# Kernel tuning notes

Hardware: AMD Instinct MI355X
Metric: run time of the kernel (lower is better)

Reference implementation:

```python
import jax, jax.numpy as jnp
import numpy as np

N_NODES = 170
SEQ = 12
BATCH = 32
D_MODEL = 120
N_HEADS = 8
FF_DIM = 2048
K_CHEB = 3  # K=2 -> K+1 = 3 polynomial orders
LN_EPS = 1e-5


def _layer_norm(x, g, b):
    m = jnp.mean(x, -1, keepdims=True)
    v = jnp.mean((x - m) ** 2, -1, keepdims=True)
    return (x - m) * jax.lax.rsqrt(v + LN_EPS) * g + b


def _graph_learn(adj, beta, w1, w2, cw, cb):
    # learned antisymmetric adjacency + 1x1-conv gating + double sym-normalization
    n = adj.shape[0]
    eps = 0.5 / n
    new = jax.nn.relu(w1 @ w2.T - w2 @ w1.T + jnp.diag(beta))
    gate = jax.nn.sigmoid(cw[0] * new + cw[1] * adj + cb)  # Conv2d(2,1,1) == weighted sum
    a = gate * new + (1.0 - gate) * adj
    d = jax.lax.rsqrt(jnp.sum(a, 1))
    a = jax.nn.relu(d[:, None] * a * d[None, :] - eps)
    d = jax.lax.rsqrt(jnp.sum(a, 1))
    return d[:, None] * a * d[None, :]


def _cheb_conv(x2d, graph, w, b):
    # x2d: (B*T, N, C); graph: (N, N); w: (K, C, O); b: (O,)
    n = graph.shape[0]
    d = jax.lax.rsqrt(jnp.sum(graph, -1))
    eye = jnp.eye(n, dtype=x2d.dtype)
    L = eye - d[:, None] * graph * d[None, :]
    Ts = [eye, L]
    for _ in range(w.shape[0] - 2):
        Ts.append(2.0 * (L @ Ts[-1]) - Ts[-2])
    T = jnp.stack(Ts)  # (K, N, N)
    h = jnp.einsum('knm,bmc->kbnc', T, x2d)
    return jnp.einsum('kbnc,kco->bno', h, w) + b


def setup_inputs() -> dict:
    key = jax.random.key(0)
    ks = jax.random.split(key, 16)
    D, F = D_MODEL, FF_DIM
    kaiming = 1.0 / np.sqrt(D)  # kaiming_uniform(a=sqrt(5)) bound for fan_in=D
    xavier = float(np.sqrt(2.0 / (D + D)))
    return {
        'x': jax.random.normal(ks[0], (BATCH, SEQ, N_NODES, D), jnp.float32),
        'adj': jax.random.uniform(ks[1], (N_NODES, N_NODES), jnp.float32),
        # GraphLearn params, stacked for Q/K/V branches (leading dim 3)
        'gl_beta': jax.random.uniform(ks[2], (3, N_NODES), jnp.float32),
        'gl_w1': jax.random.uniform(ks[3], (3, N_NODES, D), jnp.float32, -kaiming, kaiming),
        'gl_w2': jax.random.uniform(ks[4], (3, N_NODES, D), jnp.float32, -kaiming, kaiming),
        'gl_cw': jax.random.normal(ks[5], (3, 2), jnp.float32) * 0.5,
        'gl_cb': jnp.zeros((3,), jnp.float32),
        # ChebConv params per branch
        'cheb_w': jax.random.normal(ks[6], (3, K_CHEB, D, D), jnp.float32) * xavier,
        'cheb_b': jnp.zeros((3, D), jnp.float32),
        # output projection + FFN + layernorms
        'out_w': jax.random.normal(ks[7], (D, D), jnp.float32) / np.sqrt(D),
        'out_b': jnp.zeros((D,), jnp.float32),
        'ff_w1': jax.random.normal(ks[8], (D, F), jnp.float32) / np.sqrt(D),
        'ff_b1': jnp.zeros((F,), jnp.float32),
        'ff_w2': jax.random.normal(ks[9], (F, D), jnp.float32) / np.sqrt(F),
        'ff_b2': jnp.zeros((D,), jnp.float32),
        'ln1_g': jnp.ones((D,), jnp.float32),
        'ln1_b': jnp.zeros((D,), jnp.float32),
        'ln2_g': jnp.ones((D,), jnp.float32),
        'ln2_b': jnp.zeros((D,), jnp.float32),
    }


def reference(x, adj, gl_beta, gl_w1, gl_w2, gl_cw, gl_cb, cheb_w, cheb_b,
              out_w, out_b, ff_w1, ff_b1, ff_w2, ff_b2, ln1_g, ln1_b, ln2_g, ln2_b):
    B, T, N, D = x.shape
    H = N_HEADS
    hd = D // H
    x2d = x.reshape(B * T, N, D)
    qkv = []
    for i in range(3):  # Q, K, V branches (structurally distinct params)
        g = _graph_learn(adj, gl_beta[i], gl_w1[i], gl_w2[i], gl_cw[i], gl_cb[i])
        g = jax.lax.stop_gradient(g)  # torch code does graph.clone().detach()
        h = jax.nn.relu(_cheb_conv(x2d, g, cheb_w[i], cheb_b[i]))
        qkv.append(h.reshape(B, T, N, D))
    q, k, v = qkv

    def to_heads(t):  # (B,T,N,D) -> (B,N,T,H,hd)
        return t.transpose(0, 2, 1, 3).reshape(B, N, T, H, hd)
    q, k, v = to_heads(q), to_heads(k), to_heads(v)
    scores = jnp.einsum('bnqhd,bnkhd->bnhqk', q, k) / (hd ** 0.5)
    attn = jax.nn.softmax(scores, axis=-1)
    o = jnp.einsum('bnhqk,bnkhd->bnqhd', attn, v).reshape(B, N, T, D)
    o = o @ out_w + out_b  # (B,N,T,D)
    out = _layer_norm(x + o.transpose(0, 2, 1, 3), ln1_g, ln1_b)  # residual in (B,T,N,D)
    ff = jax.nn.relu(out @ ff_w1 + ff_b1) @ ff_w2 + ff_b2
    out = _layer_norm(out + ff, ln2_g, ln2_b)
    return out
```

## Files before the change

### kernel.cpp

```cpp
#include <hip/hip_runtime.h>
#include <cstddef>
#include <cstdint>

#define N_NODES 170
#define SEQ 12
#define BATCH 32
#define DM 120
#define BT (BATCH*SEQ)
#define ROWS (BT*N_NODES)
#define FF 2048

typedef short short8 __attribute__((ext_vector_type(8)));
typedef float f32x4 __attribute__((ext_vector_type(4)));

static constexpr size_t OFF_A    = 0;
static constexpr size_t OFF_G    = 86704;
static constexpr size_t OFF_A2   = 173408;
static constexpr size_t OFF_L    = 260112;
static constexpr size_t OFF_RS1  = 307824;
static constexpr size_t OFF_RS2  = 308336;
static constexpr size_t OFF_RS3  = 308848;
static constexpr size_t OFF_XT   = 309360;
static constexpr size_t OFF_XNM  = OFF_XT  + 4325376;
static constexpr size_t OFF_Y1T  = OFF_XNM + 4177920;
static constexpr size_t OFF_YNM  = OFF_Y1T + 3*4325376;
static constexpr size_t OFF_BC   = OFF_YNM + 3*8355840;
static constexpr size_t OFF_HQ   = OFF_XT;
static constexpr size_t OFF_HK   = OFF_Y1T;
static constexpr size_t OFF_HV   = OFF_Y1T + 4177920;
static constexpr size_t OFF_W1T  = OFF_YNM;
static constexpr size_t OFF_W2R  = OFF_W1T + 131072;
static constexpr size_t OFF_ONM  = OFF_W2R + 131072;
static constexpr size_t OFF_LN1  = OFF_ONM + 4177920;
static constexpr size_t OFF_LN1B = OFF_LN1 + 7833600;
static constexpr size_t OFF_OWT  = OFF_LN1B + 4177920;

static constexpr size_t Y1T_BR_STRIDE = 8650752;
static constexpr size_t YNM_BR_STRIDE = 16711680;

__device__ __forceinline__ unsigned short f2bf(float f) {
    unsigned int u = __float_as_uint(f);
    unsigned int r = (u + 0x7fffu + ((u >> 16) & 1u)) >> 16;
    return (unsigned short)r;
}
__device__ __forceinline__ float bf2f(unsigned short h) {
    return __uint_as_float(((unsigned int)h) << 16);
}
__device__ __forceinline__ void gld16(const void* g, void* l) {
    __builtin_amdgcn_global_load_lds(
        (const __attribute__((address_space(1))) void*)g,
        (__attribute__((address_space(3))) void*)l, 16, 0, 0);
}
__device__ __forceinline__ uint4 pack8(const unsigned short v[8]) {
    uint4 q;
    q.x = (unsigned)v[0] | ((unsigned)v[1] << 16);
    q.y = (unsigned)v[2] | ((unsigned)v[3] << 16);
    q.z = (unsigned)v[4] | ((unsigned)v[5] << 16);
    q.w = (unsigned)v[6] | ((unsigned)v[7] << 16);
    return q;
}

__global__ __launch_bounds__(256)
void k_gl1(const float* __restrict__ adj, const float* __restrict__ beta,
           const float* __restrict__ w1, const float* __restrict__ w2,
           const float* __restrict__ cw, const float* __restrict__ cb,
           float* __restrict__ a_out, float* __restrict__ rs_out) {
    int i  = blockIdx.x;
    int br = blockIdx.y;
    __shared__ float w1r[DM], w2r[DM];
    __shared__ float red[256];
    int tid = threadIdx.x;
    const float* w1b = w1 + (size_t)br * N_NODES * DM;
    const float* w2b = w2 + (size_t)br * N_NODES * DM;
    if (tid < DM) {
        w1r[tid] = w1b[(size_t)i * DM + tid];
        w2r[tid] = w2b[(size_t)i * DM + tid];
    }
    __syncthreads();
    float aval = 0.f;
    if (tid < N_NODES) {
        int j = tid;
        const float4* w1j = (const float4*)(w1b + (size_t)j * DM);
        const float4* w2j = (const float4*)(w2b + (size_t)j * DM);
        float s1 = 0.f, s2 = 0.f;
#pragma unroll 6
        for (int cc = 0; cc < DM / 4; ++cc) {
            float4 u = w2j[cc];
            float4 v = w1j[cc];
            s1 += w1r[cc*4+0]*u.x + w1r[cc*4+1]*u.y + w1r[cc*4+2]*u.z + w1r[cc*4+3]*u.w;
            s2 += w2r[cc*4+0]*v.x + w2r[cc*4+1]*v.y + w2r[cc*4+2]*v.z + w2r[cc*4+3]*v.w;
        }
        float nv = s1 - s2 + (j == i ? beta[br * N_NODES + i] : 0.f);
        nv = fmaxf(nv, 0.f);
        float adjv = adj[(size_t)i * N_NODES + j];
        float z = cw[br*2+0] * nv + cw[br*2+1] * adjv + cb[br];
        float gate = 1.f / (1.f + __expf(-z));
        aval = gate * nv + (1.f - gate) * adjv;
        a_out[((size_t)br * N_NODES + i) * N_NODES + j] = aval;
    }
    red[tid] = aval;
    __syncthreads();
    for (int s = 128; s > 0; s >>= 1) {
        if (tid < s) red[tid] += red[tid + s];
        __syncthreads();
    }
    if (tid == 0) rs_out[br * N_NODES + i] = red[0];
}

__global__ __launch_bounds__(256)
void k_glnorm(const float* __restrict__ in, const float* __restrict__ rs,
              float* __restrict__ out, float* __restrict__ rs_out, int mode) {
    int i  = blockIdx.x;
    int br = blockIdx.y;
    __shared__ float red[256];
    int tid = threadIdx.x;
    float di = rsqrtf(rs[br * N_NODES + i]);
    float contrib = 0.f;
    if (tid < N_NODES) {
        float dj = rsqrtf(rs[br * N_NODES + tid]);
        float v = di * in[((size_t)br * N_NODES + i) * N_NODES + tid] * dj;
        float o;
        if (mode == 2) { o = fmaxf(v - 0.5f / 170.f, 0.f); contrib = o; }
        else           { o = v; contrib = v; }
        out[((size_t)br * N_NODES + i) * N_NODES + tid] = o;
    }
    red[tid] = contrib;
    __syncthreads();
    for (int s = 128; s > 0; s >>= 1) {
        if (tid < s) red[tid] += red[tid + s];
        __syncthreads();
    }
    if (tid == 0) rs_out[br * N_NODES + i] = red[0];
}

__global__ __launch_bounds__(192)
void k_prep_L(const float* __restrict__ g_buf, const float* __restrict__ rs3,
              unsigned short* __restrict__ Lbf) {
    int i  = blockIdx.x;
    int br = blockIdx.y;
    int j  = threadIdx.x;
    if (j >= 180) return;
    float v = 0.f;
    if (i < N_NODES && j < N_NODES) {
        float di = rsqrtf(rs3[br * N_NODES + i]);
        float dj = rsqrtf(rs3[br * N_NODES + j]);
        float gg = g_buf[((size_t)br * N_NODES + i) * N_NODES + j];
        v = (i == j ? 1.f : 0.f) - di * gg * dj;
    }
    Lbf[(size_t)br * 31808 + i * 180 + j] = f2bf(v);
}

__global__ __launch_bounds__(256)
void k_prep_x(const float* __restrict__ x, unsigned short* __restrict__ xTF,
              unsigned short* __restrict__ xnm) {
    __shared__ unsigned short LX[170 * 121 + 8];
    int bt = blockIdx.x, tid = threadIdx.x;
    const float* xb = x + (size_t)bt * N_NODES * DM;
    for (int u = tid; u < 170 * 30; u += 256) {
        int nn = u / 30, cq = u - nn * 30;
        float4 v = *(const float4*)&xb[nn * 120 + cq * 4];
        LX[nn * 121 + cq * 4 + 0] = f2bf(v.x);
        LX[nn * 121 + cq * 4 + 1] = f2bf(v.y);
        LX[nn * 121 + cq * 4 + 2] = f2bf(v.z);
        LX[nn * 121 + cq * 4 + 3] = f2bf(v.w);
    }
    __syncthreads();
    for (int u = tid; u < 128 * 22; u += 256) {
        int c = u / 22, mb = u - c * 22;
        unsigned short vals[8];
#pragma unroll
        for (int i2 = 0; i2 < 8; ++i2) {
            int m = mb * 8 + i2;
            vals[i2] = (c < 120 && m < 170) ? LX[m * 121 + c] : (unsigned short)0;
        }
        *(uint4*)&xTF[(size_t)bt * 22528 + ((size_t)mb * 128 + c) * 8] = pack8(vals);
    }
    for (int u = tid; u < 170 * 16; u += 256) {
        int nn = u >> 4, b = u & 15;
        unsigned int row = bt * 170 + nn;
        unsigned short vals[8];
#pragma unroll
        for (int i2 = 0; i2 < 8; ++i2) {
            int c = b * 8 + i2;
            vals[i2] = (c < 120) ? LX[nn * 121 + c] : (unsigned short)0;
        }
        int bs = (b & 8) | ((b & 7) ^ (row & 7));
        *(uint4*)&xnm[(size_t)row * 128 + bs * 8] = pack8(vals);
    }
}

__global__ __launch_bounds__(256)
void k_prep_Bc(const float* __restrict__ cheb_w, unsigned short* __restrict__ Bc) {
    int idx = blockIdx.x * 256 + threadIdx.x;
    int br  = idx / 49152;
    int rem = idx - br * 49152;
    int o   = rem / 384;
    int c   = rem - o * 384;
    float v = 0.f;
    if (o < 120) {
        int part = c >> 7, cc = c & 127;
        if (cc < 120) {
            const float* Wb = cheb_w + (size_t)br * 3 * 14400;
            if (part == 0)      v = Wb[cc * 120 + o] - Wb[2 * 14400 + cc * 120 + o];
            else if (part == 1) v = Wb[14400 + cc * 120 + o];
            else                v = 2.f * Wb[2 * 14400 + cc * 120 + o];
        }
    }
    Bc[(size_t)br * 49152 + (((size_t)(c >> 3) * 128 + o) << 3) + (c & 7)] = f2bf(v);
}

__global__ __launch_bounds__(256)
void k_lapplyT(const unsigned short* __restrict__ Asrc_base, size_t asrc_br_stride,
               const unsigned short* __restrict__ Lg_base,
               unsigned short* __restrict__ yT_base,
               unsigned short* __restrict__ ynm_base, int coloff) {
    __shared__ __attribute__((aligned(16))) unsigned short Llds[31744];
    const int tid = threadIdx.x, w = tid >> 6, lane = tid & 63;
    const int g = lane >> 4, l15 = lane & 15;
    const int bt = blockIdx.x, br = blockIdx.y;
    const unsigned short* Asrc = Asrc_base + (size_t)br * asrc_br_stride + (size_t)bt * 22528;
    const unsigned short* Lg   = Lg_base + (size_t)br * 31808;
    unsigned short* ynm = ynm_base + (size_t)br * YNM_BR_STRIDE;
    unsigned short* yT  = yT_base ? yT_base + (size_t)br * Y1T_BR_STRIDE + (size_t)bt * 22528 : nullptr;
    const char* Lgb = (const char*)Lg;
    char* Lldsb = (char*)Llds;
#pragma unroll
    for (int it = 0; it < 16; ++it) {
        int q = it * 4 + w;
        if (q * 1024 < 63360)
            gld16(Lgb + q * 1024 + lane * 16, Lldsb + q * 1024);
    }
    short8 af[2][6];
#pragma unroll
    for (int ct2 = 0; ct2 < 2; ++ct2) {
        int c = (w * 2 + ct2) * 16 + l15;
#pragma unroll
        for (int kb = 0; kb < 6; ++kb) {
            if (kb < 5) af[ct2][kb] = *(const short8*)&Asrc[(((size_t)(kb * 4 + g)) * 128 + c) * 8];
            else {
                short8 z = {};
                af[ct2][kb] = (g < 2) ? *(const short8*)&Asrc[(((size_t)(20 + g)) * 128 + c) * 8] : z;
            }
        }
    }
    __syncthreads();
    f32x4 acc[2][11];
#pragma unroll
    for (int a = 0; a < 2; ++a)
#pragma unroll
        for (int b = 0; b < 11; ++b) acc[a][b] = (f32x4){0.f, 0.f, 0.f, 0.f};
#pragma unroll
    for (int kb = 0; kb < 6; ++kb) {
#pragma unroll
        for (int nt = 0; nt < 11; ++nt) {
            short8 bf;
            int rb = (nt * 16 + l15) * 180;
            if (kb < 5) bf = *(const short8*)&Llds[rb + kb * 32 + g * 8];
            else {
                short8 z = {};
                bf = (g < 2) ? *(const short8*)&Llds[rb + 160 + g * 8] : z;
            }
            acc[0][nt] = __builtin_amdgcn_mfma_f32_16x16x32_bf16(af[0][kb], bf, acc[0][nt], 0, 0, 0);
            acc[1][nt] = __builtin_amdgcn_mfma_f32_16x16x32_bf16(af[1][kb], bf, acc[1][nt], 0, 0, 0);
        }
    }
#pragma unroll
    for (int nt = 0; nt < 11; ++nt) {
        int nn = nt * 16 + l15;
#pragma unroll
        for (int ct2 = 0; ct2 < 2; ++ct2) {
            int base_c = (w * 2 + ct2) * 16 + g * 4;
            if (yT) {
                int f = nn >> 3, j = nn & 7;
#pragma unroll
                for (int r = 0; r < 4; ++r) {
                    int c = base_c + r;
                    float v = (c < 120 && nn < 170) ? acc[ct2][nt][r] : 0.f;
                    yT[(((size_t)f * 128 + c) << 3) + j] = f2bf(v);
                }
            }
            if (nn < 170) {
                unsigned int row = bt * 170 + nn;
                unsigned short u[4];
#pragma unroll
                for (int r = 0; r < 4; ++r)
                    u[r] = (base_c + r < 120) ? f2bf(acc[ct2][nt][r]) : (unsigned short)0;
                int bc  = coloff + base_c;
                int blk = bc >> 3;
                int bsw = (blk & 24) | ((blk & 7) ^ (row & 7));
                uint2 pk;
                pk.x = (unsigned)u[0] | ((unsigned)u[1] << 16);
                pk.y = (unsigned)u[2] | ((unsigned)u[3] << 16);
                *(uint2*)&ynm[(size_t)row * 256 + bsw * 8 + (bc & 7)] = pk;
            }
        }
    }
}

__global__ __launch_bounds__(256)
void k_combine_mfma(const unsigned short* __restrict__ xnm,
                    const unsigned short* __restrict__ ynm_base,
                    const unsigned short* __restrict__ Bc_base,
                    const float* __restrict__ bias_base,
                    unsigned short* __restrict__ h0,
                    unsigned short* __restrict__ h1,
                    unsigned short* __restrict__ h2) {
    __shared__ __attribute__((aligned(16))) unsigned short AsX[64 * 128];
    __shared__ __attribute__((aligned(16))) unsigned short AsY[64 * 256];
    const int tid = threadIdx.x, w = tid >> 6, lane = tid & 63;
    const int g = lane >> 4, l15 = lane & 15;
    const int r0 = blockIdx.x * 64;
    const int br = blockIdx.y;
    const unsigned short* ynm = ynm_base + (size_t)br * YNM_BR_STRIDE;
    const unsigned short* Bc  = Bc_base + (size_t)br * 49152;
    const float* bias = bias_base + br * DM;
    unsigned short* Hout = (br == 0) ? h0 : (br == 1) ? h1 : h2;
#pragma unroll
    for (int it = 0; it < 4; ++it) {
        int q = w * 4 + it;
        gld16(xnm + (size_t)r0 * 128 + q * 512 + lane * 8, &AsX[q * 512]);
    }
#pragma unroll
    for (int it = 0; it < 8; ++it) {
        int q = w * 8 + it;
        gld16(ynm + (size_t)r0 * 256 + q * 512 + lane * 8, &AsY[q * 512]);
    }
    __syncthreads();
    const int lr = w * 16 + l15;
    short8 af[12];
#pragma unroll
    for (int kb = 0; kb < 4; ++kb) {
        int b = kb * 4 + g;
        int bs = (b & 8) | ((b & 7) ^ (lr & 7));
        af[kb] = *(const short8*)&AsX[lr * 128 + bs * 8];
    }
#pragma unroll
    for (int kb = 4; kb < 12; ++kb) {
        int b = (kb - 4) * 4 + g;
        int bs = (b & 24) | ((b & 7) ^ (lr & 7));
        af[kb] = *(const short8*)&AsY[lr * 256 + bs * 8];
    }
    f32x4 acc[8];
#pragma unroll
    for (int c = 0; c < 8; ++c) acc[c] = (f32x4){0.f, 0.f, 0.f, 0.f};
    short8 bfA[8], bfB[8];
#pragma unroll
    for (int c = 0; c < 8; ++c)
        bfA[c] = *(const short8*)&Bc[(((size_t)g) * 128 + c * 16 + l15) * 8];
#pragma unroll
    for (int kb = 0; kb < 12; ++kb) {
        if (kb + 1 < 12) {
#pragma unroll
            for (int c = 0; c < 8; ++c) {
                short8 v = *(const short8*)&Bc[(((size_t)((kb + 1) * 4 + g)) * 128 + c * 16 + l15) * 8];
                if (kb & 1) bfA[c] = v; else bfB[c] = v;
            }
        }
#pragma unroll
        for (int c = 0; c < 8; ++c)
            acc[c] = __builtin_amdgcn_mfma_f32_16x16x32_bf16(af[kb], (kb & 1) ? bfB[c] : bfA[c], acc[c], 0, 0, 0);
    }
#pragma unroll
    for (int c = 0; c < 8; ++c) {
        int o = c * 16 + l15;
        float bv = (o < 120) ? bias[o] : 0.f;
#pragma unroll
        for (int r = 0; r < 4; ++r) {
            int row = r0 + w * 16 + g * 4 + r;
            float v = (o < 120) ? fmaxf(acc[c][r] + bv, 0.f) : 0.f;
            Hout[(size_t)row * 128 + o] = f2bf(v);
        }
    }
}

#define QP 136
__global__ __launch_bounds__(192)
void k_attn_qkv(const unsigned short* __restrict__ hq, const unsigned short* __restrict__ hk,
                const unsigned short* __restrict__ hv, unsigned short* __restrict__ onm) {
    __shared__ unsigned short qs[2][SEQ][QP], ks[2][SEQ][QP], vs[2][SEQ][QP], os[2][SEQ][QP];
    const int tid = threadIdx.x;
    const int np = blockIdx.x, b = blockIdx.y;
    for (int u = tid; u < 2 * SEQ * 16; u += 192) {
        int node = u / (SEQ * 16);
        int rem = u - node * SEQ * 16;
        int t = rem >> 4, seg = rem & 15;
        int n = np * 2 + node;
        size_t row = ((size_t)(b * SEQ + t) * N_NODES + n);
        *(uint4*)&qs[node][t][seg * 8] = *(const uint4*)&hq[row * 128 + seg * 8];
        *(uint4*)&ks[node][t][seg * 8] = *(const uint4*)&hk[row * 128 + seg * 8];
        *(uint4*)&vs[node][t][seg * 8] = *(const uint4*)&hv[row * 128 + seg * 8];
    }
    __syncthreads();
    {
        const int node = tid / 96, sub = tid % 96;
        const int h = sub & 7, tq = sub >> 3;
        float qr[15];
#pragma unroll
        for (int d = 0; d < 15; ++d) qr[d] = bf2f(qs[node][tq][h * 15 + d]);
        float sc[SEQ];
        float mx = -1e30f;
#pragma unroll
        for (int tk = 0; tk < SEQ; ++tk) {
            float s = 0.f;
#pragma unroll
            for (int d = 0; d < 15; ++d) s += qr[d] * bf2f(ks[node][tk][h * 15 + d]);
            s *= 0.25819888974716113f;
            sc[tk] = s;
            mx = fmaxf(mx, s);
        }
        float sum = 0.f;
#pragma unroll
        for (int tk = 0; tk < SEQ; ++tk) { sc[tk] = __expf(sc[tk] - mx); sum += sc[tk]; }
        float inv = 1.f / sum;
#pragma unroll
        for (int d = 0; d < 15; ++d) {
            float o = 0.f;
#pragma unroll
            for (int tk = 0; tk < SEQ; ++tk) o += sc[tk] * bf2f(vs[node][tk][h * 15 + d]);
            os[node][tq][h * 15 + d] = f2bf(o * inv);
        }
    }
    if (tid < 2 * SEQ) {
        int node = tid / SEQ, t = tid % SEQ;
#pragma unroll
        for (int j = 0; j < 8; ++j) os[node][t][120 + j] = 0;
    }
    __syncthreads();
    for (int u = tid; u < 2 * SEQ * 16; u += 192) {
        int node = u / (SEQ * 16);
        int rem = u - node * SEQ * 16;
        int t = rem >> 4, seg = rem & 15;
        int n = np * 2 + node;
        unsigned int row = (b * SEQ + t) * N_NODES + n;
        int bs = (seg & 8) | ((seg & 7) ^ (row & 7));
        *(uint4*)&onm[(size_t)row * 128 + bs * 8] = *(const uint4*)&os[node][t][seg * 8];
    }
}

__global__ __launch_bounds__(256)
void k_prep_ow(const float* __restrict__ out_w, unsigned short* __restrict__ OwT) {
    int idx = blockIdx.x * 256 + threadIdx.x;
    int o = idx >> 7, c = idx & 127;
    float v = (o < 120 && c < 120) ? out_w[(size_t)c * 120 + o] : 0.f;
    OwT[(((size_t)(c >> 3) * 128 + o) << 3) + (c & 7)] = f2bf(v);
}

__global__ __launch_bounds__(256)
void k_outproj(const unsigned short* __restrict__ onm, const unsigned short* __restrict__ OwT,
               const float* __restrict__ outb, const float* __restrict__ x,
               const float* __restrict__ g1, const float* __restrict__ be1,
               float* __restrict__ ln1, unsigned short* __restrict__ ln1bf) {
    __shared__ __attribute__((aligned(16))) unsigned short As[64 * 128];
    const int tid = threadIdx.x, w = tid >> 6, lane = tid & 63;
    const int g = lane >> 4, l15 = lane & 15;
    const int r0 = blockIdx.x * 64;
#pragma unroll
    for (int it = 0; it < 4; ++it) {
        int q = w * 4 + it;
        gld16(onm + (size_t)r0 * 128 + q * 512 + lane * 8, &As[q * 512]);
    }
    __syncthreads();
    const int lr = w * 16 + l15;
    short8 af[4];
#pragma unroll
    for (int kb = 0; kb < 4; ++kb) {
        int b = kb * 4 + g;
        int bs = (b & 8) | ((b & 7) ^ (lr & 7));
        af[kb] = *(const short8*)&As[lr * 128 + bs * 8];
    }
    f32x4 acc[8];
#pragma unroll
    for (int c = 0; c < 8; ++c) acc[c] = (f32x4){0.f, 0.f, 0.f, 0.f};
#pragma unroll
    for (int kb = 0; kb < 4; ++kb) {
#pragma unroll
        for (int c = 0; c < 8; ++c) {
            short8 bf = *(const short8*)&OwT[(((size_t)(kb * 4 + g)) * 128 + c * 16 + l15) * 8];
            acc[c] = __builtin_amdgcn_mfma_f32_16x16x32_bf16(af[kb], bf, acc[c], 0, 0, 0);
        }
    }
#pragma unroll
    for (int r = 0; r < 4; ++r) {
        int row = w * 16 + g * 4 + r;
        size_t grow = (size_t)(r0 + row);
        float vals[8];
        float s = 0.f, q = 0.f;
#pragma unroll
        for (int c = 0; c < 8; ++c) {
            int col = c * 16 + l15;
            float v = 0.f;
            if (col < DM) v = acc[c][r] + outb[col] + x[grow * DM + col];
            vals[c] = v;
            s += v; q += v * v;
        }
#pragma unroll
        for (int m = 1; m < 16; m <<= 1) {
            s += __shfl_xor(s, m);
            q += __shfl_xor(q, m);
        }
        float mean = s * (1.f / DM);
        float var  = q * (1.f / DM) - mean * mean;
        float rstd = rsqrtf(var + 1e-5f);
#pragma unroll
        for (int c = 0; c < 8; ++c) {
            int col = c * 16 + l15;
            float o = (vals[c] - mean) * rstd * ((col < DM) ? g1[col] : 0.f) + ((col < DM) ? be1[col] : 0.f);
            if (col < DM) ln1[grow * DM + col] = o;
            ln1bf[grow * 128 + col] = (col < DM) ? f2bf(o) : (unsigned short)0;
        }
    }
}

__global__ __launch_bounds__(256)
void k_prep_w1(const float* __restrict__ W1, unsigned short* __restrict__ W1T) {
    int idx = blockIdx.x * 256 + threadIdx.x;
    int o = idx >> 7, k = idx & 127;
    int b = k >> 3, ki = k & 7;
    int pos = (((b ^ (o & 7)) << 3) | ki);
    float v = (k < DM) ? W1[(size_t)k * FF + o] : 0.f;
    W1T[(size_t)o * 128 + pos] = f2bf(v);
}
__global__ __launch_bounds__(256)
void k_prep_w2(const float* __restrict__ W2, unsigned short* __restrict__ W2R) {
    int idx = blockIdx.x * 256 + threadIdx.x;
    int c = idx >> 13;
    int o = (idx >> 6) & 127;
    int j = idx & 63;
    int b = j >> 3, ji = j & 7;
    int pos = (((b ^ (o & 7)) << 3) | ji);
    float v = (o < DM) ? W2[(size_t)(c * 64 + j) * DM + o] : 0.f;
    W2R[((size_t)c << 13) + (o << 6) + pos] = f2bf(v);
}

#define LDS_XW1A 0
#define LDS_W1B  8192
#define LDS_W2A  16384
#define LDS_W2B  24576
#define LDS_HS   32768
__global__ __launch_bounds__(256, 2)
void k_ffn_mfma(const unsigned short* __restrict__ Xbf,
                const float* __restrict__ ln1,
                const unsigned short* __restrict__ W1T,
                const float* __restrict__ b1,
                const unsigned short* __restrict__ W2R,
                const float* __restrict__ b2,
                const float* __restrict__ g2, const float* __restrict__ be2,
                float* __restrict__ Out) {
    __shared__ unsigned short lds[37376];
    const int tid  = threadIdx.x;
    const int w    = tid >> 6;
    const int lane = tid & 63;
    const int g    = lane >> 4;
    const int l15  = lane & 15;
    const int r0   = blockIdx.x * 64;
    {
        const unsigned short* xsrc = Xbf + (size_t)r0 * 128;
#pragma unroll
        for (int it = 0; it < 4; ++it) {
            int seg = w * 4 + it;
            gld16(xsrc + seg * 512 + lane * 8, &lds[LDS_XW1A + seg * 512]);
        }
#pragma unroll
        for (int it = 0; it < 4; ++it) {
            int seg = w * 4 + it;
            gld16(W1T + seg * 512 + lane * 8, &lds[LDS_W1B + seg * 512]);
        }
#pragma unroll
        for (int it = 0; it < 4; ++it) {
            int seg = w * 4 + it;
            gld16(W2R + seg * 512 + lane * 8, &lds[LDS_W2A + seg * 512]);
        }
    }
    __syncthreads();
    short8 xfrag[4][4];
#pragma unroll
    for (int rt = 0; rt < 4; ++rt)
#pragma unroll
        for (int kk = 0; kk < 4; ++kk)
            xfrag[rt][kk] = *(const short8*)&lds[LDS_XW1A + (rt * 16 + l15) * 128 + kk * 32 + g * 8];

    f32x4 accO[8] = {};
    const int mycolA = w * 16 + l15;
    const int myrowB = w * 16 + l15;

    for (int t = 0; t < 32; ++t) {
        __syncthreads();
        const int p = t & 1;
        if (t + 1 < 32) {
            const unsigned short* w1src = W1T + (size_t)(t + 1) * 8192;
            const unsigned short* w2src = W2R + (size_t)(t + 1) * 8192;
            unsigned short* w1dst = &lds[(p ? LDS_W1B : LDS_XW1A)];
            unsigned short* w2dst = &lds[(p ? LDS_W2A : LDS_W2B)];
#pragma unroll
            for (int it = 0; it < 4; ++it) {
                int seg = w * 4 + it;
                gld16(w1src + seg * 512 + lane * 8, w1dst + seg * 512);
                gld16(w2src + seg * 512 + lane * 8, w2dst + seg * 512);
            }
        }
        {
            const unsigned short* w1p = &lds[p ? LDS_XW1A : LDS_W1B];
            f32x4 accA[4] = {};
#pragma unroll
            for (int kk = 0; kk < 4; ++kk) {
                int b = kk * 4 + g;
                short8 bfrag = *(const short8*)&w1p[mycolA * 128 + ((b ^ (mycolA & 7)) << 3)];
#pragma unroll
                for (int rt = 0; rt < 4; ++rt)
                    accA[rt] = __builtin_amdgcn_mfma_f32_16x16x32_bf16(xfrag[rt][kk], bfrag, accA[rt], 0, 0, 0);
            }
            float b1v = b1[t * 64 + mycolA];
#pragma unroll
            for (int rt = 0; rt < 4; ++rt)
#pragma unroll
                for (int r = 0; r < 4; ++r) {
                    float v = fmaxf(accA[rt][r] + b1v, 0.f);
                    lds[LDS_HS + (rt * 16 + g * 4 + r) * 72 + mycolA] = f2bf(v);
                }
        }
        asm volatile("s_waitcnt lgkmcnt(0)" ::: "memory");
        __builtin_amdgcn_sched_barrier(0);
        __builtin_amdgcn_s_barrier();
        {
            const unsigned short* w2p = &lds[p ? LDS_W2B : LDS_W2A];
#pragma unroll
            for (int kk = 0; kk < 2; ++kk) {
                short8 hfrag = *(const short8*)&lds[LDS_HS + myrowB * 72 + kk * 32 + g * 8];
                int b = kk * 4 + g;
#pragma unroll
                for (int c = 0; c < 8; ++c) {
                    int o = c * 16 + l15;
                    short8 w2frag = *(const short8*)&w2p[(o << 6) + ((b ^ (o & 7)) << 3)];
                    accO[c] = __builtin_amdgcn_mfma_f32_16x16x32_bf16(hfrag, w2frag, accO[c], 0, 0, 0);
                }
            }
        }
    }
#pragma unroll
    for (int r = 0; r < 4; ++r) {
        int row = w * 16 + g * 4 + r;
        size_t grow = (size_t)(r0 + row);
        float vals[8];
        float s = 0.f, q = 0.f;
#pragma unroll
        for (int c = 0; c < 8; ++c) {
            int col = c * 16 + l15;
            float v = 0.f;
            if (col < DM) v = accO[c][r] + b2[col] + ln1[grow * DM + col];
            vals[c] = v;
            s += v; q += v * v;
        }
#pragma unroll
        for (int m = 1; m < 16; m <<= 1) {
            s += __shfl_xor(s, m);
            q += __shfl_xor(q, m);
        }
        float mean = s * (1.f / DM);
        float var  = q * (1.f / DM) - mean * mean;
        float rstd = rsqrtf(var + 1e-5f);
#pragma unroll
        for (int c = 0; c < 8; ++c) {
            int col = c * 16 + l15;
            if (col < DM)
                Out[grow * DM + col] = (vals[c] - mean) * rstd * g2[col] + be2[col];
        }
    }
}

extern "C" void kernel_launch(void* const* d_in, const int* in_sizes, int n_in,
                              void* d_out, int out_size, void* d_ws, size_t ws_size,
                              hipStream_t stream) {
    const float* x      = (const float*)d_in[0];
    const float* adj    = (const float*)d_in[1];
    const float* gl_beta= (const float*)d_in[2];
    const float* gl_w1  = (const float*)d_in[3];
    const float* gl_w2  = (const float*)d_in[4];
    const float* gl_cw  = (const float*)d_in[5];
    const float* gl_cb  = (const float*)d_in[6];
    const float* cheb_w = (const float*)d_in[7];
    const float* cheb_b = (const float*)d_in[8];
    const float* out_w  = (const float*)d_in[9];
    const float* out_b  = (const float*)d_in[10];
    const float* ff_w1  = (const float*)d_in[11];
    const float* ff_b1  = (const float*)d_in[12];
    const float* ff_w2  = (const float*)d_in[13];
    const float* ff_b2  = (const float*)d_in[14];
    const float* ln1_g  = (const float*)d_in[15];
    const float* ln1_b  = (const float*)d_in[16];
    const float* ln2_g  = (const float*)d_in[17];
    const float* ln2_b  = (const float*)d_in[18];

    float* ws    = (float*)d_ws;
    float* a_buf = ws + OFF_A;
    float* g_buf = ws + OFF_G;
    float* a2buf = ws + OFF_A2;
    float* rs1   = ws + OFF_RS1;
    float* rs2   = ws + OFF_RS2;
    float* rs3   = ws + OFF_RS3;
    unsigned short* L_bf = (unsigned short*)(ws + OFF_L);
    unsigned short* xT   = (unsigned short*)(ws + OFF_XT);
    unsigned short* xnm  = (unsigned short*)(ws + OFF_XNM);
    unsigned short* y1T  = (unsigned short*)(ws + OFF_Y1T);
    unsigned short* ynm  = (unsigned short*)(ws + OFF_YNM);
    unsigned short* Bc   = (unsigned short*)(ws + OFF_BC);
    unsigned short* hq   = (unsigned short*)(ws + OFF_HQ);
    unsigned short* hk   = (unsigned short*)(ws + OFF_HK);
    unsigned short* hv   = (unsigned short*)(ws + OFF_HV);
    unsigned short* W1T  = (unsigned short*)(ws + OFF_W1T);
    unsigned short* W2R  = (unsigned short*)(ws + OFF_W2R);
    unsigned short* onm  = (unsigned short*)(ws + OFF_ONM);
    float*          ln1  = ws + OFF_LN1;
    unsigned short* ln1bf= (unsigned short*)(ws + OFF_LN1B);
    unsigned short* OwT  = (unsigned short*)(ws + OFF_OWT);

    k_gl1   <<<dim3(N_NODES, 3), 256, 0, stream>>>(adj, gl_beta, gl_w1, gl_w2, gl_cw, gl_cb, a_buf, rs1);
    k_glnorm<<<dim3(N_NODES, 3), 256, 0, stream>>>(a_buf, rs1, a2buf, rs2, 2);
    k_glnorm<<<dim3(N_NODES, 3), 256, 0, stream>>>(a2buf, rs2, g_buf, rs3, 3);
    k_prep_L<<<dim3(176, 3), 192, 0, stream>>>(g_buf, rs3, L_bf);

    k_prep_x <<<BT, 256, 0, stream>>>(x, xT, xnm);
    k_prep_Bc<<<576, 256, 0, stream>>>(cheb_w, Bc);

    k_lapplyT<<<dim3(BT, 3), 256, 0, stream>>>(xT, 0, L_bf, y1T, ynm, 0);
    k_lapplyT<<<dim3(BT, 3), 256, 0, stream>>>(y1T, Y1T_BR_STRIDE, L_bf, nullptr, ynm, 128);

    k_combine_mfma<<<dim3(ROWS / 64, 3), 256, 0, stream>>>(xnm, ynm, Bc, cheb_b, hq, hk, hv);

    k_prep_w1<<<(2048 * 128) / 256, 256, 0, stream>>>(ff_w1, W1T);
    k_prep_w2<<<(32 * 128 * 64) / 256, 256, 0, stream>>>(ff_w2, W2R);
    k_prep_ow<<<64, 256, 0, stream>>>(out_w, OwT);

    k_attn_qkv<<<dim3(N_NODES / 2, BATCH), 192, 0, stream>>>(hq, hk, hv, onm);

    k_outproj<<<ROWS / 64, 256, 0, stream>>>(onm, OwT, out_b, x, ln1_g, ln1_b, ln1, ln1bf);

    k_ffn_mfma<<<ROWS / 64, 256, 0, stream>>>(ln1bf, ln1, W1T, ff_b1, W2R, ff_b2, ln2_g, ln2_b, (float*)d_out);
}
```

Measured before the change: 457.6 us.

## Fuse two Laplacian hops into one kernel and merge weight-prep launches

The two Chebyshev Laplacian-apply passes are merged into one kernel. The first-hop result stays in shared memory and is fed back as the A operand for the second hop, so the global y1T intermediate is no longer written and re-read. The four weight-prep kernels are combined into a single launch, and the FFN first GEMM swaps its MFMA operands so the bias can be loaded as a float4 and hidden activations stored as packed uint2. The cost is more shared memory per block (an extra 128x184 bf16 buffer), which may lower occupancy, and the workspace layout is reshuffled.

```diff
diff --git a/kernel.cpp b/kernel.cpp
--- a/kernel.cpp
+++ b/kernel.cpp
@@ -22,20 +22,18 @@
 static constexpr size_t OFF_RS3  = 308848;
 static constexpr size_t OFF_XT   = 309360;
 static constexpr size_t OFF_XNM  = OFF_XT  + 4325376;
-static constexpr size_t OFF_Y1T  = OFF_XNM + 4177920;
-static constexpr size_t OFF_YNM  = OFF_Y1T + 3*4325376;
+static constexpr size_t OFF_HK   = OFF_XNM + 4177920;
+static constexpr size_t OFF_HV   = OFF_HK  + 4177920;
+static constexpr size_t OFF_YNM  = OFF_HV  + 4177920;
 static constexpr size_t OFF_BC   = OFF_YNM + 3*8355840;
+static constexpr size_t OFF_W1T  = OFF_BC  + 73728;
+static constexpr size_t OFF_W2R  = OFF_W1T + 131072;
+static constexpr size_t OFF_OWT  = OFF_W2R + 131072;
 static constexpr size_t OFF_HQ   = OFF_XT;
-static constexpr size_t OFF_HK   = OFF_Y1T;
-static constexpr size_t OFF_HV   = OFF_Y1T + 4177920;
-static constexpr size_t OFF_W1T  = OFF_YNM;
-static constexpr size_t OFF_W2R  = OFF_W1T + 131072;
-static constexpr size_t OFF_ONM  = OFF_W2R + 131072;
+static constexpr size_t OFF_ONM  = OFF_YNM;
 static constexpr size_t OFF_LN1  = OFF_ONM + 4177920;
 static constexpr size_t OFF_LN1B = OFF_LN1 + 7833600;
-static constexpr size_t OFF_OWT  = OFF_LN1B + 4177920;
-
-static constexpr size_t Y1T_BR_STRIDE = 8650752;
+
 static constexpr size_t YNM_BR_STRIDE = 16711680;
 
 __device__ __forceinline__ unsigned short f2bf(float f) {
@@ -190,38 +188,64 @@
 }
 
 __global__ __launch_bounds__(256)
-void k_prep_Bc(const float* __restrict__ cheb_w, unsigned short* __restrict__ Bc) {
+void k_prep_weights(const float* __restrict__ ff_w1, const float* __restrict__ ff_w2,
+                    const float* __restrict__ out_w, const float* __restrict__ cheb_w,
+                    unsigned short* __restrict__ W1T, unsigned short* __restrict__ W2R,
+                    unsigned short* __restrict__ OwT, unsigned short* __restrict__ Bc) {
     int idx = blockIdx.x * 256 + threadIdx.x;
-    int br  = idx / 49152;
-    int rem = idx - br * 49152;
-    int o   = rem / 384;
-    int c   = rem - o * 384;
-    float v = 0.f;
-    if (o < 120) {
-        int part = c >> 7, cc = c & 127;
-        if (cc < 120) {
-            const float* Wb = cheb_w + (size_t)br * 3 * 14400;
-            if (part == 0)      v = Wb[cc * 120 + o] - Wb[2 * 14400 + cc * 120 + o];
-            else if (part == 1) v = Wb[14400 + cc * 120 + o];
-            else                v = 2.f * Wb[2 * 14400 + cc * 120 + o];
-        }
-    }
-    Bc[(size_t)br * 49152 + (((size_t)(c >> 3) * 128 + o) << 3) + (c & 7)] = f2bf(v);
-}
-
+    if (idx < 262144) {
+        int o = idx >> 7, k = idx & 127;
+        int b = k >> 3, ki = k & 7;
+        int pos = (((b ^ (o & 7)) << 3) | ki);
+        float v = (k < DM) ? ff_w1[(size_t)k * FF + o] : 0.f;
+        W1T[(size_t)o * 128 + pos] = f2bf(v);
+    } else if (idx < 524288) {
+        int i = idx - 262144;
+        int c = i >> 13;
+        int o = (i >> 6) & 127;
+        int j = i & 63;
+        int b = j >> 3, ji = j & 7;
+        int pos = (((b ^ (o & 7)) << 3) | ji);
+        float v = (o < DM) ? ff_w2[(size_t)(c * 64 + j) * DM + o] : 0.f;
+        W2R[((size_t)c << 13) + (o << 6) + pos] = f2bf(v);
+    } else if (idx < 540672) {
+        int i = idx - 524288;
+        int o = i >> 7, c = i & 127;
+        float v = (o < 120 && c < 120) ? out_w[(size_t)c * 120 + o] : 0.f;
+        OwT[(((size_t)(c >> 3) * 128 + o) << 3) + (c & 7)] = f2bf(v);
+    } else {
+        int i = idx - 540672;
+        int br  = i / 49152;
+        int rem = i - br * 49152;
+        int o   = rem / 384;
+        int c   = rem - o * 384;
+        float v = 0.f;
+        if (o < 120) {
+            int part = c >> 7, cc = c & 127;
+            if (cc < 120) {
+                const float* Wb = cheb_w + (size_t)br * 3 * 14400;
+                if (part == 0)      v = Wb[cc * 120 + o] - Wb[2 * 14400 + cc * 120 + o];
+                else if (part == 1) v = Wb[14400 + cc * 120 + o];
+                else                v = 2.f * Wb[2 * 14400 + cc * 120 + o];
+            }
+        }
+        Bc[(size_t)br * 49152 + (((size_t)(c >> 3) * 128 + o) << 3) + (c & 7)] = f2bf(v);
+    }
+}
+
+#define MP 184
 __global__ __launch_bounds__(256)
-void k_lapplyT(const unsigned short* __restrict__ Asrc_base, size_t asrc_br_stride,
+void k_lapply2(const unsigned short* __restrict__ xTg,
                const unsigned short* __restrict__ Lg_base,
-               unsigned short* __restrict__ yT_base,
-               unsigned short* __restrict__ ynm_base, int coloff) {
+               unsigned short* __restrict__ ynm_base) {
     __shared__ __attribute__((aligned(16))) unsigned short Llds[31744];
+    __shared__ __attribute__((aligned(16))) unsigned short Y1[128 * MP];
     const int tid = threadIdx.x, w = tid >> 6, lane = tid & 63;
     const int g = lane >> 4, l15 = lane & 15;
     const int bt = blockIdx.x, br = blockIdx.y;
-    const unsigned short* Asrc = Asrc_base + (size_t)br * asrc_br_stride + (size_t)bt * 22528;
+    const unsigned short* Asrc = xTg + (size_t)bt * 22528;
     const unsigned short* Lg   = Lg_base + (size_t)br * 31808;
     unsigned short* ynm = ynm_base + (size_t)br * YNM_BR_STRIDE;
-    unsigned short* yT  = yT_base ? yT_base + (size_t)br * Y1T_BR_STRIDE + (size_t)bt * 22528 : nullptr;
     const char* Lgb = (const char*)Lg;
     char* Lldsb = (char*)Llds;
 #pragma unroll
@@ -245,53 +269,68 @@
     }
     __syncthreads();
     f32x4 acc[2][11];
-#pragma unroll
-    for (int a = 0; a < 2; ++a)
-#pragma unroll
-        for (int b = 0; b < 11; ++b) acc[a][b] = (f32x4){0.f, 0.f, 0.f, 0.f};
-#pragma unroll
-    for (int kb = 0; kb < 6; ++kb) {
+
+    for (int hop = 0; hop < 2; ++hop) {
+#pragma unroll
+        for (int a = 0; a < 2; ++a)
+#pragma unroll
+            for (int b = 0; b < 11; ++b) acc[a][b] = (f32x4){0.f, 0.f, 0.f, 0.f};
+#pragma unroll
+        for (int kb = 0; kb < 6; ++kb) {
+#pragma unroll
+            for (int nt = 0; nt < 11; ++nt) {
+                short8 bf;
+                int rb = (nt * 16 + l15) * 180;
+                if (kb < 5) bf = *(const short8*)&Llds[rb + kb * 32 + g * 8];
+                else {
+                    short8 z = {};
+                    bf = (g < 2) ? *(const short8*)&Llds[rb + 160 + g * 8] : z;
+                }
+                acc[0][nt] = __builtin_amdgcn_mfma_f32_16x16x32_bf16(af[0][kb], bf, acc[0][nt], 0, 0, 0);
+                acc[1][nt] = __builtin_amdgcn_mfma_f32_16x16x32_bf16(af[1][kb], bf, acc[1][nt], 0, 0, 0);
+            }
+        }
+        const int coloff = hop * 128;
 #pragma unroll
         for (int nt = 0; nt < 11; ++nt) {
-            short8 bf;
-            int rb = (nt * 16 + l15) * 180;
-            if (kb < 5) bf = *(const short8*)&Llds[rb + kb * 32 + g * 8];
-            else {
-                short8 z = {};
-                bf = (g < 2) ? *(const short8*)&Llds[rb + 160 + g * 8] : z;
-            }
-            acc[0][nt] = __builtin_amdgcn_mfma_f32_16x16x32_bf16(af[0][kb], bf, acc[0][nt], 0, 0, 0);
-            acc[1][nt] = __builtin_amdgcn_mfma_f32_16x16x32_bf16(af[1][kb], bf, acc[1][nt], 0, 0, 0);
-        }
-    }
-#pragma unroll
-    for (int nt = 0; nt < 11; ++nt) {
-        int nn = nt * 16 + l15;
-#pragma unroll
-        for (int ct2 = 0; ct2 < 2; ++ct2) {
-            int base_c = (w * 2 + ct2) * 16 + g * 4;
-            if (yT) {
-                int f = nn >> 3, j = nn & 7;
-#pragma unroll
-                for (int r = 0; r < 4; ++r) {
-                    int c = base_c + r;
-                    float v = (c < 120 && nn < 170) ? acc[ct2][nt][r] : 0.f;
-                    yT[(((size_t)f * 128 + c) << 3) + j] = f2bf(v);
+            int nn = nt * 16 + l15;
+#pragma unroll
+            for (int ct2 = 0; ct2 < 2; ++ct2) {
+                int base_c = (w * 2 + ct2) * 16 + g * 4;
+                if (hop == 0) {
+#pragma unroll
+                    for (int r = 0; r < 4; ++r)
+                        Y1[(base_c + r) * MP + nn] = f2bf(acc[ct2][nt][r]);
                 }
-            }
-            if (nn < 170) {
-                unsigned int row = bt * 170 + nn;
-                unsigned short u[4];
-#pragma unroll
-                for (int r = 0; r < 4; ++r)
-                    u[r] = (base_c + r < 120) ? f2bf(acc[ct2][nt][r]) : (unsigned short)0;
-                int bc  = coloff + base_c;
-                int blk = bc >> 3;
-                int bsw = (blk & 24) | ((blk & 7) ^ (row & 7));
-                uint2 pk;
-                pk.x = (unsigned)u[0] | ((unsigned)u[1] << 16);
-                pk.y = (unsigned)u[2] | ((unsigned)u[3] << 16);
-                *(uint2*)&ynm[(size_t)row * 256 + bsw * 8 + (bc & 7)] = pk;
+                if (nn < 170) {
+                    unsigned int row = bt * 170 + nn;
+                    unsigned short u[4];
+#pragma unroll
+                    for (int r = 0; r < 4; ++r)
+                        u[r] = (base_c + r < 120) ? f2bf(acc[ct2][nt][r]) : (unsigned short)0;
+                    int bc  = coloff + base_c;
+                    int blk = bc >> 3;
+                    int bsw = (blk & 24) | ((blk & 7) ^ (row & 7));
+                    uint2 pk;
+                    pk.x = (unsigned)u[0] | ((unsigned)u[1] << 16);
+                    pk.y = (unsigned)u[2] | ((unsigned)u[3] << 16);
+                    *(uint2*)&ynm[(size_t)row * 256 + bsw * 8 + (bc & 7)] = pk;
+                }
+            }
+        }
+        if (hop == 0) {
+            __syncthreads();
+#pragma unroll
+            for (int ct2 = 0; ct2 < 2; ++ct2) {
+                int c = (w * 2 + ct2) * 16 + l15;
+#pragma unroll
+                for (int kb = 0; kb < 6; ++kb) {
+                    if (kb < 5) af[ct2][kb] = *(const short8*)&Y1[c * MP + kb * 32 + g * 8];
+                    else {
+                        short8 z = {};
+                        af[ct2][kb] = (g < 2) ? *(const short8*)&Y1[c * MP + 160 + g * 8] : z;
+                    }
+                }
             }
         }
     }
@@ -438,14 +477,6 @@
 }
 
 __global__ __launch_bounds__(256)
-void k_prep_ow(const float* __restrict__ out_w, unsigned short* __restrict__ OwT) {
-    int idx = blockIdx.x * 256 + threadIdx.x;
-    int o = idx >> 7, c = idx & 127;
-    float v = (o < 120 && c < 120) ? out_w[(size_t)c * 120 + o] : 0.f;
-    OwT[(((size_t)(c >> 3) * 128 + o) << 3) + (c & 7)] = f2bf(v);
-}
-
-__global__ __launch_bounds__(256)
 void k_outproj(const unsigned short* __restrict__ onm, const unsigned short* __restrict__ OwT,
                const float* __restrict__ outb, const float* __restrict__ x,
                const float* __restrict__ g1, const float* __restrict__ be1,
@@ -509,27 +540,6 @@
             ln1bf[grow * 128 + col] = (col < DM) ? f2bf(o) : (unsigned short)0;
         }
     }
-}
-
-__global__ __launch_bounds__(256)
-void k_prep_w1(const float* __restrict__ W1, unsigned short* __restrict__ W1T) {
-    int idx = blockIdx.x * 256 + threadIdx.x;
-    int o = idx >> 7, k = idx & 127;
-    int b = k >> 3, ki = k & 7;
-    int pos = (((b ^ (o & 7)) << 3) | ki);
-    float v = (k < DM) ? W1[(size_t)k * FF + o] : 0.f;
-    W1T[(size_t)o * 128 + pos] = f2bf(v);
-}
-__global__ __launch_bounds__(256)
-void k_prep_w2(const float* __restrict__ W2, unsigned short* __restrict__ W2R) {
-    int idx = blockIdx.x * 256 + threadIdx.x;
-    int c = idx >> 13;
-    int o = (idx >> 6) & 127;
-    int j = idx & 63;
-    int b = j >> 3, ji = j & 7;
-    int pos = (((b ^ (o & 7)) << 3) | ji);
-    float v = (o < DM) ? W2[(size_t)(c * 64 + j) * DM + o] : 0.f;
-    W2R[((size_t)c << 13) + (o << 6) + pos] = f2bf(v);
 }
 
 #define LDS_XW1A 0
@@ -607,16 +617,21 @@
                 short8 bfrag = *(const short8*)&w1p[mycolA * 128 + ((b ^ (mycolA & 7)) << 3)];
 #pragma unroll
                 for (int rt = 0; rt < 4; ++rt)
-                    accA[rt] = __builtin_amdgcn_mfma_f32_16x16x32_bf16(xfrag[rt][kk], bfrag, accA[rt], 0, 0, 0);
-            }
-            float b1v = b1[t * 64 + mycolA];
-#pragma unroll
-            for (int rt = 0; rt < 4; ++rt)
-#pragma unroll
-                for (int r = 0; r < 4; ++r) {
-                    float v = fmaxf(accA[rt][r] + b1v, 0.f);
-                    lds[LDS_HS + (rt * 16 + g * 4 + r) * 72 + mycolA] = f2bf(v);
-                }
+                    accA[rt] = __builtin_amdgcn_mfma_f32_16x16x32_bf16(bfrag, xfrag[rt][kk], accA[rt], 0, 0, 0);
+            }
+            float4 b4 = *(const float4*)&b1[t * 64 + w * 16 + g * 4];
+            float bb[4] = {b4.x, b4.y, b4.z, b4.w};
+#pragma unroll
+            for (int rt = 0; rt < 4; ++rt) {
+                unsigned short u[4];
+#pragma unroll
+                for (int r = 0; r < 4; ++r)
+                    u[r] = f2bf(fmaxf(accA[rt][r] + bb[r], 0.f));
+                uint2 pk;
+                pk.x = (unsigned)u[0] | ((unsigned)u[1] << 16);
+                pk.y = (unsigned)u[2] | ((unsigned)u[3] << 16);
+                *(uint2*)&lds[LDS_HS + (rt * 16 + l15) * 72 + w * 16 + g * 4] = pk;
+            }
         }
         asm volatile("s_waitcnt lgkmcnt(0)" ::: "memory");
         __builtin_amdgcn_sched_barrier(0);
@@ -700,7 +715,6 @@
     unsigned short* L_bf = (unsigned short*)(ws + OFF_L);
     unsigned short* xT   = (unsigned short*)(ws + OFF_XT);
     unsigned short* xnm  = (unsigned short*)(ws + OFF_XNM);
-    unsigned short* y1T  = (unsigned short*)(ws + OFF_Y1T);
     unsigned short* ynm  = (unsigned short*)(ws + OFF_YNM);
     unsigned short* Bc   = (unsigned short*)(ws + OFF_BC);
     unsigned short* hq   = (unsigned short*)(ws + OFF_HQ);
@@ -708,28 +722,24 @@
     unsigned short* hv   = (unsigned short*)(ws + OFF_HV);
     unsigned short* W1T  = (unsigned short*)(ws + OFF_W1T);
     unsigned short* W2R  = (unsigned short*)(ws + OFF_W2R);
+    unsigned short* OwT  = (unsigned short*)(ws + OFF_OWT);
     unsigned short* onm  = (unsigned short*)(ws + OFF_ONM);
     float*          ln1  = ws + OFF_LN1;
     unsigned short* ln1bf= (unsigned short*)(ws + OFF_LN1B);
-    unsigned short* OwT  = (unsigned short*)(ws + OFF_OWT);
+
+    k_prep_weights<<<2688, 256, 0, stream>>>(ff_w1, ff_w2, out_w, cheb_w, W1T, W2R, OwT, Bc);
 
     k_gl1   <<<dim3(N_NODES, 3), 256, 0, stream>>>(adj, gl_beta, gl_w1, gl_w2, gl_cw, gl_cb, a_buf, rs1);
     k_glnorm<<<dim3(N_NODES, 3), 256, 0, stream>>>(a_buf, rs1, a2buf, rs2, 2);
     k_glnorm<<<dim3(N_NODES, 3), 256, 0, stream>>>(a2buf, rs2, g_buf, rs3, 3);
     k_prep_L<<<dim3(176, 3), 192, 0, stream>>>(g_buf, rs3, L_bf);
 
-    k_prep_x <<<BT, 256, 0, stream>>>(x, xT, xnm);
-    k_prep_Bc<<<576, 256, 0, stream>>>(cheb_w, Bc);
-
-    k_lapplyT<<<dim3(BT, 3), 256, 0, stream>>>(xT, 0, L_bf, y1T, ynm, 0);
-    k_lapplyT<<<dim3(BT, 3), 256, 0, stream>>>(y1T, Y1T_BR_STRIDE, L_bf, nullptr, ynm, 128);
+    k_prep_x<<<BT, 256, 0, stream>>>(x, xT, xnm);
+
+    k_lapply2<<<dim3(BT, 3), 256, 0, stream>>>(xT, L_bf, ynm);
 
     k_combine_mfma<<<dim3(ROWS / 64, 3), 256, 0, stream>>>(xnm, ynm, Bc, cheb_b, hq, hk, hv);
 
-    k_prep_w1<<<(2048 * 128) / 256, 256, 0, stream>>>(ff_w1, W1T);
-    k_prep_w2<<<(32 * 128 * 64) / 256, 256, 0, stream>>>(ff_w2, W2R);
-    k_prep_ow<<<64, 256, 0, stream>>>(out_w, OwT);
-
     k_attn_qkv<<<dim3(N_NODES / 2, BATCH), 192, 0, stream>>>(hq, hk, hv, onm);
 
     k_outproj<<<ROWS / 64, 256, 0, stream>>>(onm, OwT, out_b, x, ln1_g, ln1_b, ln1, ln1bf);
```

After: 446.6 us. 1.02x faster.
